# Kernel optimization log

Measured on AMD Instinct MI355X. Metric: run time of the kernel, lower is better.

The kernel has to match this reference:

```python
import jax, jax.numpy as jnp
import numpy as np

B, C, H, W, KS = 64, 128, 36, 100, 9
WSCALE = 0.02  # < 1/sqrt(C*KS) to keep the additive recurrence stable


def setup_inputs() -> dict:
    key = jax.random.key(0)
    kx, kd, ku, kr, kl = jax.random.split(key, 5)
    return {
        "x": jax.random.normal(kx, (B, C, H, W), dtype=jnp.float32),
        "w_d": jax.random.normal(kd, (C, C, KS), dtype=jnp.float32) * WSCALE,
        "w_u": jax.random.normal(ku, (C, C, KS), dtype=jnp.float32) * WSCALE,
        "w_r": jax.random.normal(kr, (C, C, KS), dtype=jnp.float32) * WSCALE,
        "w_l": jax.random.normal(kl, (C, C, KS), dtype=jnp.float32) * WSCALE,
    }


def _conv1d(z, w):
    # z: [B, C, L], w: [Cout, Cin, ks], SAME padding (matches padding=ks//2, bias=False)
    ks = w.shape[-1]
    return jax.lax.conv_general_dilated(
        z, w, window_strides=(1,), padding=[(ks // 2, ks // 2)],
        dimension_numbers=("NCH", "OIH", "NCH"))


def _scan_dir(x, w, axis, reverse):
    # singleDURL: out[0] = slice[0]; out[i] = slice[i] + relu(conv(out[i-1]))
    xs = jnp.moveaxis(x, axis, 0)  # [L, B, C, M]
    if reverse:
        xs = xs[::-1]

    def step(carry, s):
        nxt = s + jax.nn.relu(_conv1d(carry, w))
        return nxt, nxt

    _, outs = jax.lax.scan(step, xs[0], xs[1:])
    outs = jnp.concatenate([xs[:1], outs], axis=0)
    if reverse:
        outs = outs[::-1]
    return jnp.moveaxis(outs, 0, axis)


def reference(x, w_d, w_u, w_r, w_l):
    # allDURL: D (down, scan over H, 1xks conv over W), U (up), R (right, scan over W,
    # ksx1 conv over H), L (left)
    x = _scan_dir(x, w_d, axis=2, reverse=False)
    x = _scan_dir(x, w_u, axis=2, reverse=True)
    x = _scan_dir(x, w_r, axis=3, reverse=False)
    x = _scan_dir(x, w_l, axis=3, reverse=True)
    return x
```

## Files before the change

kernel.cpp:

```cpp
#include <hip/hip_runtime.h>

#define Bn 64
#define Cn 128
#define Hn 36
#define Wn 100
#define KSn 9

#define B_STRIDE (Cn * Hn * Wn)
#define C_STRIDE (Hn * Wn)

#define WH_CHUNK 80
#define WW_CHUNK 40
#define WH_SIZE (16 * Cn * WH_CHUNK)
#define WW_SIZE (32 * Cn * WW_CHUNK)

__global__ void __launch_bounds__(256) k_copy(const float4* __restrict__ s,
                                              float4* __restrict__ d, int n4) {
  int i = blockIdx.x * 256 + threadIdx.x;
  if (i < n4) d[i] = s[i];
}

__global__ void __launch_bounds__(256) k_prep_h(const float* __restrict__ w,
                                                float* __restrict__ o) {
  int i = blockIdx.x * 256 + threadIdx.x;
  if (i >= 16 * Cn * 72) return;
  int k = i % 9, j = (i / 9) % 8, ci = (i / 72) % Cn, cog = i / (72 * Cn);
  o[(cog * Cn + ci) * WH_CHUNK + j * 9 + k] = w[((cog * 8 + j) * Cn + ci) * KSn + k];
}
__global__ void __launch_bounds__(256) k_prep_w(const float* __restrict__ w,
                                                float* __restrict__ o) {
  int i = blockIdx.x * 256 + threadIdx.x;
  if (i >= 32 * Cn * 36) return;
  int k = i % 9, j = (i / 9) % 4, ci = (i / 36) % Cn, coq = i / (36 * Cn);
  o[(coq * Cn + ci) * WW_CHUNK + j * 9 + k] = w[((coq * 4 + j) * Cn + ci) * KSn + k];
}

__global__ void __launch_bounds__(256) k_hstep2(float* __restrict__ buf,
                                                const float* __restrict__ wp,
                                                int hp, int hc) {
  __shared__ float prev[Cn][Wn + 8];
  const int b = blockIdx.x;
  const int t = threadIdx.x;

  const float* rb = buf + ((size_t)b * Cn * Hn + hp) * Wn;
  for (int g = t; g < Cn * (Wn / 4); g += 256) {
    int ci = g / 25, wq = g % 25;
    float4 v = *(const float4*)(rb + (size_t)ci * C_STRIDE + wq * 4);
    *(float4*)&prev[ci][4 + wq * 4] = v;
  }
  for (int g = t; g < Cn * 8; g += 256) {
    int ci = g >> 3, s = g & 7;
    prev[ci][(s < 4) ? s : (Wn + s)] = 0.f;
  }
  __syncthreads();

  const int w = t & 127;
  if (w >= Wn) return;
  const int cog = blockIdx.y * 2 + __builtin_amdgcn_readfirstlane(t >> 7);

  float acc[8] = {0.f, 0.f, 0.f, 0.f, 0.f, 0.f, 0.f, 0.f};
  const float* wb = wp + (size_t)cog * Cn * WH_CHUNK;
#pragma unroll 2
  for (int ci = 0; ci < Cn; ++ci) {
    float p[KSn];
#pragma unroll
    for (int k = 0; k < KSn; ++k) p[k] = prev[ci][w + k];
    const float* wr = wb + ci * WH_CHUNK;
#pragma unroll
    for (int j = 0; j < 8; ++j)
#pragma unroll
      for (int k = 0; k < KSn; ++k) acc[j] = fmaf(p[k], wr[j * 9 + k], acc[j]);
  }
  float* ob = buf + ((size_t)(b * Cn + cog * 8) * Hn + hc) * Wn + w;
#pragma unroll
  for (int j = 0; j < 8; ++j) ob[(size_t)j * C_STRIDE] += fmaxf(acc[j], 0.f);
}

__global__ void __launch_bounds__(256) k_wstep2(float* __restrict__ tb,
                                                const float* __restrict__ wp,
                                                int wpos, int wc) {
  __shared__ float prev[Cn][Hn + 8];
  const int b = blockIdx.x;
  const int t = threadIdx.x;

  const float* cb = tb + ((size_t)b * Cn * Wn + wpos) * Hn;
  for (int g = t; g < Cn * (Hn / 4); g += 256) {
    int ci = g / 9, hq = g % 9;
    float4 v = *(const float4*)(cb + (size_t)ci * C_STRIDE + hq * 4);
    *(float4*)&prev[ci][4 + hq * 4] = v;
  }
  for (int g = t; g < Cn * 8; g += 256) {
    int ci = g >> 3, s = g & 7;
    prev[ci][(s < 4) ? s : (Hn + s)] = 0.f;
  }
  __syncthreads();

  const int h = t & 63;
  if (h >= Hn) return;
  const int coq = blockIdx.y * 4 + __builtin_amdgcn_readfirstlane(t >> 6);

  float acc[4] = {0.f, 0.f, 0.f, 0.f};
  const float* wb = wp + (size_t)coq * Cn * WW_CHUNK;
#pragma unroll 2
  for (int ci = 0; ci < Cn; ++ci) {
    float p[KSn];
#pragma unroll
    for (int k = 0; k < KSn; ++k) p[k] = prev[ci][h + k];
    const float* wr = wb + ci * WW_CHUNK;
#pragma unroll
    for (int j = 0; j < 4; ++j)
#pragma unroll
      for (int k = 0; k < KSn; ++k) acc[j] = fmaf(p[k], wr[j * 9 + k], acc[j]);
  }
  float* ob = tb + ((size_t)(b * Cn + coq * 4) * Wn + wc) * Hn + h;
#pragma unroll
  for (int j = 0; j < 4; ++j) ob[(size_t)j * C_STRIDE] += fmaxf(acc[j], 0.f);
}

__global__ void __launch_bounds__(256) k_t_hw2wh(const float* __restrict__ in,
                                                 float* __restrict__ out) {
  __shared__ float tile[Hn][Wn + 1];
  const int bc = blockIdx.x;
  const float* ib = in + (size_t)bc * C_STRIDE;
  float* ob = out + (size_t)bc * C_STRIDE;
  for (int f = threadIdx.x; f < Hn * Wn; f += 256) tile[f / Wn][f % Wn] = ib[f];
  __syncthreads();
  for (int f = threadIdx.x; f < Hn * Wn; f += 256) {
    int w = f / Hn, h = f % Hn;
    ob[f] = tile[h][w];
  }
}
__global__ void __launch_bounds__(256) k_t_wh2hw(const float* __restrict__ in,
                                                 float* __restrict__ out) {
  __shared__ float tile[Hn][Wn + 1];
  const int bc = blockIdx.x;
  const float* ib = in + (size_t)bc * C_STRIDE;
  float* ob = out + (size_t)bc * C_STRIDE;
  for (int f = threadIdx.x; f < Hn * Wn; f += 256) {
    int w = f / Hn, h = f % Hn;
    tile[h][w] = ib[f];
  }
  __syncthreads();
  for (int f = threadIdx.x; f < Hn * Wn; f += 256) ob[f] = tile[f / Wn][f % Wn];
}

__global__ void __launch_bounds__(128) k_hstep(float* __restrict__ buf,
                                               const float* __restrict__ wt,
                                               int hp, int hc) {
  __shared__ float prev[Cn][Wn + 8];
  const int b = blockIdx.x;
  const int cog = blockIdx.y;
  const int t = threadIdx.x;
  const float* rb = buf + ((size_t)b * Cn * Hn + hp) * Wn;
  for (int g = t; g < Cn * (Wn / 4); g += 128) {
    int ci = g / 25, wq = g % 25;
    float4 v = *(const float4*)(rb + (size_t)ci * C_STRIDE + wq * 4);
    *(float4*)&prev[ci][4 + wq * 4] = v;
  }
  for (int g = t; g < Cn * 8; g += 128) {
    int ci = g >> 3, s = g & 7;
    prev[ci][(s < 4) ? s : (Wn + s)] = 0.f;
  }
  __syncthreads();
  if (t >= Wn) return;
  float acc[8] = {0.f, 0.f, 0.f, 0.f, 0.f, 0.f, 0.f, 0.f};
  const float* wb = wt + (size_t)cog * 8 * Cn * KSn;
  for (int ci = 0; ci < Cn; ++ci) {
    float p[KSn];
#pragma unroll
    for (int k = 0; k < KSn; ++k) p[k] = prev[ci][t + k];
#pragma unroll
    for (int j = 0; j < 8; ++j) {
      const float* w9 = wb + ((size_t)j * Cn + ci) * KSn;
#pragma unroll
      for (int k = 0; k < KSn; ++k) acc[j] = fmaf(p[k], w9[k], acc[j]);
    }
  }
  float* ob = buf + ((size_t)(b * Cn + cog * 8) * Hn + hc) * Wn + t;
#pragma unroll
  for (int j = 0; j < 8; ++j) ob[(size_t)j * C_STRIDE] += fmaxf(acc[j], 0.f);
}
__global__ void __launch_bounds__(128) k_wstep_d(float* __restrict__ buf,
                                                 const float* __restrict__ wt,
                                                 int wpos, int wc) {
  __shared__ float prev[Cn][Hn + 8];
  const int b = blockIdx.x;
  const int cog = blockIdx.y;
  const int t = threadIdx.x;
  const int h = t & 63;
  const int jb = __builtin_amdgcn_readfirstlane((t >> 6) * 4);
  for (int g = t; g < Cn * Hn; g += 128) {
    int ci = g / Hn, hh = g % Hn;
    prev[ci][4 + hh] = buf[((size_t)(b * Cn + ci) * Hn + hh) * Wn + wpos];
  }
  for (int g = t; g < Cn * 8; g += 128) {
    int ci = g >> 3, s = g & 7;
    prev[ci][(s < 4) ? s : (Hn + s)] = 0.f;
  }
  __syncthreads();
  if (h >= Hn) return;
  float acc[4] = {0.f, 0.f, 0.f, 0.f};
  const float* wb = wt + (size_t)(cog * 8 + jb) * Cn * KSn;
  for (int ci = 0; ci < Cn; ++ci) {
    float p[KSn];
#pragma unroll
    for (int k = 0; k < KSn; ++k) p[k] = prev[ci][h + k];
#pragma unroll
    for (int j = 0; j < 4; ++j) {
      const float* w9 = wb + ((size_t)j * Cn + ci) * KSn;
#pragma unroll
      for (int k = 0; k < KSn; ++k) acc[j] = fmaf(p[k], w9[k], acc[j]);
    }
  }
  float* ob = buf + ((size_t)(b * Cn + cog * 8 + jb) * Hn + h) * Wn + wc;
#pragma unroll
  for (int j = 0; j < 4; ++j) ob[(size_t)j * C_STRIDE] += fmaxf(acc[j], 0.f);
}

extern "C" void kernel_launch(void* const* d_in, const int* in_sizes, int n_in,
                              void* d_out, int out_size, void* d_ws, size_t ws_size,
                              hipStream_t stream) {
  const float* x  = (const float*)d_in[0];
  const float* wd = (const float*)d_in[1];
  const float* wu = (const float*)d_in[2];
  const float* wr = (const float*)d_in[3];
  const float* wl = (const float*)d_in[4];
  float* buf = (float*)d_out;
  const size_t nelem = (size_t)Bn * B_STRIDE;
  const size_t need = (nelem + 2 * (size_t)WH_SIZE + 2 * (size_t)WW_SIZE) * 4;

  k_copy<<<(int)(nelem / 4 + 255) / 256, 256, 0, stream>>>(
      (const float4*)x, (float4*)buf, (int)(nelem / 4));

  if (ws_size >= need) {
    float* tb  = (float*)d_ws;
    float* pwd = tb + nelem;
    float* pwu = pwd + WH_SIZE;
    float* pwr = pwu + WH_SIZE;
    float* pwl = pwr + WW_SIZE;

    k_prep_h<<<(16 * Cn * 72 + 255) / 256, 256, 0, stream>>>(wd, pwd);
    k_prep_h<<<(16 * Cn * 72 + 255) / 256, 256, 0, stream>>>(wu, pwu);
    k_prep_w<<<(32 * Cn * 36 + 255) / 256, 256, 0, stream>>>(wr, pwr);
    k_prep_w<<<(32 * Cn * 36 + 255) / 256, 256, 0, stream>>>(wl, pwl);

    dim3 gh(Bn, Cn / 16);
    for (int hh = 1; hh < Hn; ++hh)
      k_hstep2<<<gh, 256, 0, stream>>>(buf, pwd, hh - 1, hh);
    for (int hh = Hn - 2; hh >= 0; --hh)
      k_hstep2<<<gh, 256, 0, stream>>>(buf, pwu, hh + 1, hh);

    k_t_hw2wh<<<Bn * Cn, 256, 0, stream>>>(buf, tb);
    dim3 gw(Bn, Cn / 16);
    for (int ww = 1; ww < Wn; ++ww)
      k_wstep2<<<gw, 256, 0, stream>>>(tb, pwr, ww - 1, ww);
    for (int ww = Wn - 2; ww >= 0; --ww)
      k_wstep2<<<gw, 256, 0, stream>>>(tb, pwl, ww + 1, ww);
    k_t_wh2hw<<<Bn * Cn, 256, 0, stream>>>(tb, buf);
  } else {
    dim3 g8(Bn, Cn / 8);
    for (int hh = 1; hh < Hn; ++hh)
      k_hstep<<<g8, 128, 0, stream>>>(buf, wd, hh - 1, hh);
    for (int hh = Hn - 2; hh >= 0; --hh)
      k_hstep<<<g8, 128, 0, stream>>>(buf, wu, hh + 1, hh);
    for (int ww = 1; ww < Wn; ++ww)
      k_wstep_d<<<g8, 128, 0, stream>>>(buf, wr, ww - 1, ww);
    for (int ww = Wn - 2; ww >= 0; --ww)
      k_wstep_d<<<g8, 128, 0, stream>>>(buf, wl, ww + 1, ww);
  }
}
```

Before: 10.19 ms.

## Register-tile step kernels with LDS-staged weights and split-K reduction

Rewrites the per-row and per-column recurrence step kernels so each thread computes a 4-channel by 4/5-position register tile. Weights are re-laid out once and staged in chunks through shared memory, with a register double-buffer prefetching the next chunk. The W-direction kernel also splits the input channels across the four wavefronts and reduces the partial sums through shared memory. The goal is more FMAs per load, fewer redundant global weight reads, and fewer blocks per step (grid of 64x4 instead of 64x8). In exchange it adds more __syncthreads, higher register pressure and lower parallelism per launch.

Measured after the change: 11.03 ms. 1.08x slower.

```diff
diff --git a/kernel.cpp b/kernel.cpp
--- a/kernel.cpp
+++ b/kernel.cpp
@@ -9,10 +9,7 @@
 #define B_STRIDE (Cn * Hn * Wn)
 #define C_STRIDE (Hn * Wn)
 
-#define WH_CHUNK 80
-#define WW_CHUNK 40
-#define WH_SIZE (16 * Cn * WH_CHUNK)
-#define WW_SIZE (32 * Cn * WW_CHUNK)
+#define PW_SIZE (Cn * Cn * KSn)
 
 __global__ void __launch_bounds__(256) k_copy(const float4* __restrict__ s,
                                               float4* __restrict__ d, int n4) {
@@ -20,101 +17,198 @@
   if (i < n4) d[i] = s[i];
 }
 
-__global__ void __launch_bounds__(256) k_prep_h(const float* __restrict__ w,
-                                                float* __restrict__ o) {
+__global__ void __launch_bounds__(256) k_prep3(const float* __restrict__ w,
+                                               float* __restrict__ o) {
   int i = blockIdx.x * 256 + threadIdx.x;
-  if (i >= 16 * Cn * 72) return;
-  int k = i % 9, j = (i / 9) % 8, ci = (i / 72) % Cn, cog = i / (72 * Cn);
-  o[(cog * Cn + ci) * WH_CHUNK + j * 9 + k] = w[((cog * 8 + j) * Cn + ci) * KSn + k];
-}
-__global__ void __launch_bounds__(256) k_prep_w(const float* __restrict__ w,
-                                                float* __restrict__ o) {
-  int i = blockIdx.x * 256 + threadIdx.x;
-  if (i >= 32 * Cn * 36) return;
-  int k = i % 9, j = (i / 9) % 4, ci = (i / 36) % Cn, coq = i / (36 * Cn);
-  o[(coq * Cn + ci) * WW_CHUNK + j * 9 + k] = w[((coq * 4 + j) * Cn + ci) * KSn + k];
-}
-
-__global__ void __launch_bounds__(256) k_hstep2(float* __restrict__ buf,
+  if (i >= PW_SIZE) return;
+  int k = i % 9;
+  int j = (i / 9) & 3;
+  int coset = (i / 36) & 7;
+  int ci = (i / 288) & 127;
+  int coq = i / 36864;
+  o[i] = w[((coq * 32 + coset * 4 + j) * Cn + ci) * KSn + k];
+}
+
+__global__ void __launch_bounds__(256) k_hstep3(float* __restrict__ buf,
                                                 const float* __restrict__ wp,
                                                 int hp, int hc) {
   __shared__ float prev[Cn][Wn + 8];
-  const int b = blockIdx.x;
-  const int t = threadIdx.x;
+  __shared__ float wch[8][8][36];
+  const int b = blockIdx.x, coq = blockIdx.y, t = threadIdx.x;
+  const int coset = t & 7;
+  const int wgrp = t >> 3;
+  const int w0r = wgrp * 4;
+  const int w0 = (w0r > 96) ? 96 : w0r;
 
   const float* rb = buf + ((size_t)b * Cn * Hn + hp) * Wn;
-  for (int g = t; g < Cn * (Wn / 4); g += 256) {
+  for (int g = t; g < Cn * 25; g += 256) {
     int ci = g / 25, wq = g % 25;
-    float4 v = *(const float4*)(rb + (size_t)ci * C_STRIDE + wq * 4);
-    *(float4*)&prev[ci][4 + wq * 4] = v;
+    *(float4*)&prev[ci][4 + wq * 4] = *(const float4*)(rb + (size_t)ci * C_STRIDE + wq * 4);
   }
   for (int g = t; g < Cn * 8; g += 256) {
     int ci = g >> 3, s = g & 7;
     prev[ci][(s < 4) ? s : (Wn + s)] = 0.f;
   }
-  __syncthreads();
-
-  const int w = t & 127;
-  if (w >= Wn) return;
-  const int cog = blockIdx.y * 2 + __builtin_amdgcn_readfirstlane(t >> 7);
-
-  float acc[8] = {0.f, 0.f, 0.f, 0.f, 0.f, 0.f, 0.f, 0.f};
-  const float* wb = wp + (size_t)cog * Cn * WH_CHUNK;
+
+  const float* wsrc = wp + (size_t)coq * (Cn * 288);
+  float4 wstage[3];
+  {
+    const float4* s4 = (const float4*)wsrc;
+#pragma unroll
+    for (int r = 0; r < 3; ++r) {
+      int g = t + 256 * r;
+      if (g < 576) wstage[r] = s4[g];
+    }
+  }
+
+  float acc[4][4] = {};
+  float4* d4 = (float4*)&wch[0][0][0];
+  for (int c = 0; c < 16; ++c) {
+    __syncthreads();
+#pragma unroll
+    for (int r = 0; r < 3; ++r) {
+      int g = t + 256 * r;
+      if (g < 576) d4[g] = wstage[r];
+    }
+    __syncthreads();
+    if (c < 15) {
+      const float4* s4 = (const float4*)(wsrc + (c + 1) * 2304);
+#pragma unroll
+      for (int r = 0; r < 3; ++r) {
+        int g = t + 256 * r;
+        if (g < 576) wstage[r] = s4[g];
+      }
+    }
 #pragma unroll 2
-  for (int ci = 0; ci < Cn; ++ci) {
-    float p[KSn];
-#pragma unroll
-    for (int k = 0; k < KSn; ++k) p[k] = prev[ci][w + k];
-    const float* wr = wb + ci * WH_CHUNK;
-#pragma unroll
-    for (int j = 0; j < 8; ++j)
-#pragma unroll
-      for (int k = 0; k < KSn; ++k) acc[j] = fmaf(p[k], wr[j * 9 + k], acc[j]);
-  }
-  float* ob = buf + ((size_t)(b * Cn + cog * 8) * Hn + hc) * Wn + w;
-#pragma unroll
-  for (int j = 0; j < 8; ++j) ob[(size_t)j * C_STRIDE] += fmaxf(acc[j], 0.f);
-}
-
-__global__ void __launch_bounds__(256) k_wstep2(float* __restrict__ tb,
+    for (int c8 = 0; c8 < 8; ++c8) {
+      const int ci = c * 8 + c8;
+      float p[12];
+#pragma unroll
+      for (int q = 0; q < 12; ++q) p[q] = prev[ci][w0 + q];
+      const float* wr = &wch[c8][coset][0];
+      float wreg[36];
+#pragma unroll
+      for (int r = 0; r < 36; ++r) wreg[r] = wr[r];
+#pragma unroll
+      for (int j = 0; j < 4; ++j)
+#pragma unroll
+        for (int k = 0; k < KSn; ++k) {
+          const float wv = wreg[j * 9 + k];
+#pragma unroll
+          for (int i = 0; i < 4; ++i) acc[j][i] = fmaf(p[i + k], wv, acc[j][i]);
+        }
+    }
+  }
+
+  if (w0r <= 96) {
+    float* ob = buf + ((size_t)(b * Cn + coq * 32 + coset * 4) * Hn + hc) * Wn + w0;
+#pragma unroll
+    for (int j = 0; j < 4; ++j) {
+      float4* op = (float4*)(ob + (size_t)j * C_STRIDE);
+      float4 o = *op;
+      o.x += fmaxf(acc[j][0], 0.f);
+      o.y += fmaxf(acc[j][1], 0.f);
+      o.z += fmaxf(acc[j][2], 0.f);
+      o.w += fmaxf(acc[j][3], 0.f);
+      *op = o;
+    }
+  }
+}
+
+__global__ void __launch_bounds__(256) k_wstep3(float* __restrict__ tb,
                                                 const float* __restrict__ wp,
                                                 int wpos, int wc) {
   __shared__ float prev[Cn][Hn + 8];
-  const int b = blockIdx.x;
-  const int t = threadIdx.x;
+  __shared__ float wch[4][8][8][36];
+  const int b = blockIdx.x, coq = blockIdx.y, t = threadIdx.x;
+  const int wv = t >> 6, l = t & 63;
+  const int coset = l & 7, hgrp = l >> 3;
+  const int h0r = hgrp * 5;
+  const int h0 = (h0r > 31) ? 31 : h0r;
 
   const float* cb = tb + ((size_t)b * Cn * Wn + wpos) * Hn;
-  for (int g = t; g < Cn * (Hn / 4); g += 256) {
+  for (int g = t; g < Cn * 9; g += 256) {
     int ci = g / 9, hq = g % 9;
-    float4 v = *(const float4*)(cb + (size_t)ci * C_STRIDE + hq * 4);
-    *(float4*)&prev[ci][4 + hq * 4] = v;
+    *(float4*)&prev[ci][4 + hq * 4] = *(const float4*)(cb + (size_t)ci * C_STRIDE + hq * 4);
   }
   for (int g = t; g < Cn * 8; g += 256) {
     int ci = g >> 3, s = g & 7;
     prev[ci][(s < 4) ? s : (Hn + s)] = 0.f;
   }
-  __syncthreads();
-
-  const int h = t & 63;
-  if (h >= Hn) return;
-  const int coq = blockIdx.y * 4 + __builtin_amdgcn_readfirstlane(t >> 6);
-
-  float acc[4] = {0.f, 0.f, 0.f, 0.f};
-  const float* wb = wp + (size_t)coq * Cn * WW_CHUNK;
+
+  const float* wsrc = wp + (size_t)coq * (Cn * 288);
+  float4 wstage[9];
+#pragma unroll
+  for (int r = 0; r < 9; ++r) {
+    int g = t + 256 * r;
+    int gw = g / 576, rem = g % 576;
+    wstage[r] = *((const float4*)wsrc + (size_t)(gw * 32) * 72 + rem);
+  }
+
+  float acc[4][5] = {};
+  float4* d4 = (float4*)&wch[0][0][0][0];
+  for (int c = 0; c < 4; ++c) {
+    __syncthreads();
+#pragma unroll
+    for (int r = 0; r < 9; ++r) d4[t + 256 * r] = wstage[r];
+    __syncthreads();
+    if (c < 3) {
+#pragma unroll
+      for (int r = 0; r < 9; ++r) {
+        int g = t + 256 * r;
+        int gw = g / 576, rem = g % 576;
+        wstage[r] = *((const float4*)wsrc + (size_t)(gw * 32 + (c + 1) * 8) * 72 + rem);
+      }
+    }
 #pragma unroll 2
-  for (int ci = 0; ci < Cn; ++ci) {
-    float p[KSn];
-#pragma unroll
-    for (int k = 0; k < KSn; ++k) p[k] = prev[ci][h + k];
-    const float* wr = wb + ci * WW_CHUNK;
-#pragma unroll
-    for (int j = 0; j < 4; ++j)
-#pragma unroll
-      for (int k = 0; k < KSn; ++k) acc[j] = fmaf(p[k], wr[j * 9 + k], acc[j]);
-  }
-  float* ob = tb + ((size_t)(b * Cn + coq * 4) * Wn + wc) * Hn + h;
-#pragma unroll
-  for (int j = 0; j < 4; ++j) ob[(size_t)j * C_STRIDE] += fmaxf(acc[j], 0.f);
+    for (int c8 = 0; c8 < 8; ++c8) {
+      const int ci = wv * 32 + c * 8 + c8;
+      float p[13];
+#pragma unroll
+      for (int q = 0; q < 13; ++q) p[q] = prev[ci][h0 + q];
+      const float* wr = &wch[wv][c8][coset][0];
+      float wreg[36];
+#pragma unroll
+      for (int r = 0; r < 36; ++r) wreg[r] = wr[r];
+#pragma unroll
+      for (int j = 0; j < 4; ++j)
+#pragma unroll
+        for (int k = 0; k < KSn; ++k) {
+          const float wvv = wreg[j * 9 + k];
+#pragma unroll
+          for (int i = 0; i < 5; ++i) acc[j][i] = fmaf(p[i + k], wvv, acc[j][i]);
+        }
+    }
+  }
+
+  __syncthreads();
+  float* red = &wch[0][0][0][0];
+#pragma unroll
+  for (int j = 0; j < 4; ++j)
+#pragma unroll
+    for (int i = 0; i < 5; ++i) red[(wv * 64 + l) * 20 + j * 5 + i] = acc[j][i];
+  __syncthreads();
+  {
+    const int oh = t & 7, oc = t >> 3;
+    const int rj = oc & 3, rcs = oc >> 2;
+    const int rl = oh * 8 + rcs;
+    const int oh0r = oh * 5;
+    const int oh0 = (oh0r > 31) ? 31 : oh0r;
+    float v[5];
+#pragma unroll
+    for (int i = 0; i < 5; ++i) v[i] = red[rl * 20 + rj * 5 + i];
+#pragma unroll
+    for (int w2 = 1; w2 < 4; ++w2)
+#pragma unroll
+      for (int i = 0; i < 5; ++i) v[i] += red[(w2 * 64 + rl) * 20 + rj * 5 + i];
+    const int co = coq * 32 + rcs * 4 + rj;
+    float* ob = tb + ((size_t)(b * Cn + co) * Wn + wc) * Hn;
+#pragma unroll
+    for (int i = 0; i < 5; ++i) {
+      const int h = oh0 + i;
+      if (h >= oh0r && h < Hn) ob[h] += fmaxf(v[i], 0.f);
+    }
+  }
 }
 
 __global__ void __launch_bounds__(256) k_t_hw2wh(const float* __restrict__ in,
@@ -220,6 +314,7 @@
 extern "C" void kernel_launch(void* const* d_in, const int* in_sizes, int n_in,
                               void* d_out, int out_size, void* d_ws, size_t ws_size,
                               hipStream_t stream) {
+  (void)in_sizes; (void)n_in; (void)out_size;
   const float* x  = (const float*)d_in[0];
   const float* wd = (const float*)d_in[1];
   const float* wu = (const float*)d_in[2];
@@ -227,7 +322,7 @@
   const float* wl = (const float*)d_in[4];
   float* buf = (float*)d_out;
   const size_t nelem = (size_t)Bn * B_STRIDE;
-  const size_t need = (nelem + 2 * (size_t)WH_SIZE + 2 * (size_t)WW_SIZE) * 4;
+  const size_t need = (nelem + 4 * (size_t)PW_SIZE) * 4;
 
   k_copy<<<(int)(nelem / 4 + 255) / 256, 256, 0, stream>>>(
       (const float4*)x, (float4*)buf, (int)(nelem / 4));
@@ -235,27 +330,27 @@
   if (ws_size >= need) {
     float* tb  = (float*)d_ws;
     float* pwd = tb + nelem;
-    float* pwu = pwd + WH_SIZE;
-    float* pwr = pwu + WH_SIZE;
-    float* pwl = pwr + WW_SIZE;
-
-    k_prep_h<<<(16 * Cn * 72 + 255) / 256, 256, 0, stream>>>(wd, pwd);
-    k_prep_h<<<(16 * Cn * 72 + 255) / 256, 256, 0, stream>>>(wu, pwu);
-    k_prep_w<<<(32 * Cn * 36 + 255) / 256, 256, 0, stream>>>(wr, pwr);
-    k_prep_w<<<(32 * Cn * 36 + 255) / 256, 256, 0, stream>>>(wl, pwl);
-
-    dim3 gh(Bn, Cn / 16);
+    float* pwu = pwd + PW_SIZE;
+    float* pwr = pwu + PW_SIZE;
+    float* pwl = pwr + PW_SIZE;
+
+    const int pg = (PW_SIZE + 255) / 256;
+    k_prep3<<<pg, 256, 0, stream>>>(wd, pwd);
+    k_prep3<<<pg, 256, 0, stream>>>(wu, pwu);
+    k_prep3<<<pg, 256, 0, stream>>>(wr, pwr);
+    k_prep3<<<pg, 256, 0, stream>>>(wl, pwl);
+
+    dim3 g4(Bn, 4);
     for (int hh = 1; hh < Hn; ++hh)
-      k_hstep2<<<gh, 256, 0, stream>>>(buf, pwd, hh - 1, hh);
+      k_hstep3<<<g4, 256, 0, stream>>>(buf, pwd, hh - 1, hh);
     for (int hh = Hn - 2; hh >= 0; --hh)
-      k_hstep2<<<gh, 256, 0, stream>>>(buf, pwu, hh + 1, hh);
+      k_hstep3<<<g4, 256, 0, stream>>>(buf, pwu, hh + 1, hh);
 
     k_t_hw2wh<<<Bn * Cn, 256, 0, stream>>>(buf, tb);
-    dim3 gw(Bn, Cn / 16);
     for (int ww = 1; ww < Wn; ++ww)
-      k_wstep2<<<gw, 256, 0, stream>>>(tb, pwr, ww - 1, ww);
+      k_wstep3<<<g4, 256, 0, stream>>>(tb, pwr, ww - 1, ww);
     for (int ww = Wn - 2; ww >= 0; --ww)
-      k_wstep2<<<gw, 256, 0, stream>>>(tb, pwl, ww + 1, ww);
+      k_wstep3<<<g4, 256, 0, stream>>>(tb, pwl, ww + 1, ww);
     k_t_wh2hw<<<Bn * Cn, 256, 0, stream>>>(tb, buf);
   } else {
     dim3 g8(Bn, Cn / 8);
```

## Fuse per-step scan launches into persistent kernels with per-batch atomic barriers

Applied to the files above, without the earlier changes.

Replaces the ~268 per-step kernel launches of the H and W scans with two persistent kernels of 256 blocks (512 threads each). The blocks for one batch element synchronise each step through a global atomic counter barrier. The goal is to remove launch overhead and the global sync between steps. In exchange it depends on all 256 blocks being co-resident, since the barrier would deadlock otherwise. It also lowers per-block parallelism, uses spin-wait polling, and relies on caches being coherent across workgroups.

After: 11.54 ms. 13.2% more time.

```diff
diff --git a/kernel.cpp b/kernel.cpp
--- a/kernel.cpp
+++ b/kernel.cpp
@@ -18,6 +18,11 @@
                                               float4* __restrict__ d, int n4) {
   int i = blockIdx.x * 256 + threadIdx.x;
   if (i < n4) d[i] = s[i];
+}
+
+__global__ void __launch_bounds__(256) k_zero(unsigned* p, int n) {
+  int i = blockIdx.x * 256 + threadIdx.x;
+  if (i < n) p[i] = 0u;
 }
 
 __global__ void __launch_bounds__(256) k_prep_h(const float* __restrict__ w,
@@ -35,86 +40,130 @@
   o[(coq * Cn + ci) * WW_CHUNK + j * 9 + k] = w[((coq * 4 + j) * Cn + ci) * KSn + k];
 }
 
-__global__ void __launch_bounds__(256) k_hstep2(float* __restrict__ buf,
-                                                const float* __restrict__ wp,
-                                                int hp, int hc) {
+__device__ __forceinline__ void bbar(unsigned* c, unsigned target) {
+  __syncthreads();
+  if (threadIdx.x == 0) {
+    __hip_atomic_fetch_add(c, 1u, __ATOMIC_RELEASE, __HIP_MEMORY_SCOPE_AGENT);
+    while (__hip_atomic_load(c, __ATOMIC_RELAXED, __HIP_MEMORY_SCOPE_AGENT) <
+           target)
+      __builtin_amdgcn_s_sleep(1);
+    __builtin_amdgcn_fence(__ATOMIC_ACQUIRE, "agent");
+  }
+  __syncthreads();
+}
+
+__global__ void __launch_bounds__(512, 1) k_hfused(float* __restrict__ buf,
+                                                   const float* __restrict__ pwd,
+                                                   const float* __restrict__ pwu,
+                                                   unsigned* __restrict__ ctr) {
   __shared__ float prev[Cn][Wn + 8];
-  const int b = blockIdx.x;
+  const int bid = blockIdx.x;
+  const int b = bid & 63;
+  const int coq = bid >> 6;
   const int t = threadIdx.x;
-
-  const float* rb = buf + ((size_t)b * Cn * Hn + hp) * Wn;
-  for (int g = t; g < Cn * (Wn / 4); g += 256) {
-    int ci = g / 25, wq = g % 25;
-    float4 v = *(const float4*)(rb + (size_t)ci * C_STRIDE + wq * 4);
-    *(float4*)&prev[ci][4 + wq * 4] = v;
-  }
-  for (int g = t; g < Cn * 8; g += 256) {
-    int ci = g >> 3, s = g & 7;
-    prev[ci][(s < 4) ? s : (Wn + s)] = 0.f;
-  }
-  __syncthreads();
-
   const int w = t & 127;
-  if (w >= Wn) return;
-  const int cog = blockIdx.y * 2 + __builtin_amdgcn_readfirstlane(t >> 7);
-
-  float acc[8] = {0.f, 0.f, 0.f, 0.f, 0.f, 0.f, 0.f, 0.f};
-  const float* wb = wp + (size_t)cog * Cn * WH_CHUNK;
+  const int plane = __builtin_amdgcn_readfirstlane(t >> 7);
+  const int cog = coq * 4 + plane;
+  unsigned* myc = ctr + b;
+  unsigned gen = 0;
+
+  for (int phase = 0; phase < 2; ++phase) {
+    const float* wp = phase ? pwu : pwd;
+    const float* wb = wp + (size_t)cog * Cn * WH_CHUNK;
+    for (int s = 0; s < Hn - 1; ++s) {
+      const int hc = phase ? (Hn - 2 - s) : (1 + s);
+      const int hp = phase ? (hc + 1) : (hc - 1);
+
+      const float* rb = buf + ((size_t)b * Cn * Hn + hp) * Wn;
+      for (int g = t; g < Cn * 25; g += 512) {
+        int ci = g / 25, wq = g % 25;
+        *(float4*)&prev[ci][4 + wq * 4] =
+            *(const float4*)(rb + (size_t)ci * C_STRIDE + wq * 4);
+      }
+      for (int g = t; g < Cn * 8; g += 512) {
+        int ci = g >> 3, sp = g & 7;
+        prev[ci][(sp < 4) ? sp : (Wn + sp)] = 0.f;
+      }
+      __syncthreads();
+
+      if (w < Wn) {
+        float acc[8] = {0.f, 0.f, 0.f, 0.f, 0.f, 0.f, 0.f, 0.f};
 #pragma unroll 2
-  for (int ci = 0; ci < Cn; ++ci) {
-    float p[KSn];
-#pragma unroll
-    for (int k = 0; k < KSn; ++k) p[k] = prev[ci][w + k];
-    const float* wr = wb + ci * WH_CHUNK;
-#pragma unroll
-    for (int j = 0; j < 8; ++j)
-#pragma unroll
-      for (int k = 0; k < KSn; ++k) acc[j] = fmaf(p[k], wr[j * 9 + k], acc[j]);
-  }
-  float* ob = buf + ((size_t)(b * Cn + cog * 8) * Hn + hc) * Wn + w;
-#pragma unroll
-  for (int j = 0; j < 8; ++j) ob[(size_t)j * C_STRIDE] += fmaxf(acc[j], 0.f);
-}
-
-__global__ void __launch_bounds__(256) k_wstep2(float* __restrict__ tb,
-                                                const float* __restrict__ wp,
-                                                int wpos, int wc) {
+        for (int ci = 0; ci < Cn; ++ci) {
+          float p[KSn];
+#pragma unroll
+          for (int k = 0; k < KSn; ++k) p[k] = prev[ci][w + k];
+          const float* wr = wb + ci * WH_CHUNK;
+#pragma unroll
+          for (int j = 0; j < 8; ++j)
+#pragma unroll
+            for (int k = 0; k < KSn; ++k) acc[j] = fmaf(p[k], wr[j * 9 + k], acc[j]);
+        }
+        float* ob = buf + ((size_t)(b * Cn + cog * 8) * Hn + hc) * Wn + w;
+#pragma unroll
+        for (int j = 0; j < 8; ++j) ob[(size_t)j * C_STRIDE] += fmaxf(acc[j], 0.f);
+      }
+      ++gen;
+      bbar(myc, gen * 4u);
+    }
+  }
+}
+
+__global__ void __launch_bounds__(512, 1) k_wfused(float* __restrict__ tb,
+                                                   const float* __restrict__ pwr,
+                                                   const float* __restrict__ pwl,
+                                                   unsigned* __restrict__ ctr) {
   __shared__ float prev[Cn][Hn + 8];
-  const int b = blockIdx.x;
+  const int bid = blockIdx.x;
+  const int b = bid & 63;
+  const int coq = bid >> 6;
   const int t = threadIdx.x;
-
-  const float* cb = tb + ((size_t)b * Cn * Wn + wpos) * Hn;
-  for (int g = t; g < Cn * (Hn / 4); g += 256) {
-    int ci = g / 9, hq = g % 9;
-    float4 v = *(const float4*)(cb + (size_t)ci * C_STRIDE + hq * 4);
-    *(float4*)&prev[ci][4 + hq * 4] = v;
-  }
-  for (int g = t; g < Cn * 8; g += 256) {
-    int ci = g >> 3, s = g & 7;
-    prev[ci][(s < 4) ? s : (Hn + s)] = 0.f;
-  }
-  __syncthreads();
-
   const int h = t & 63;
-  if (h >= Hn) return;
-  const int coq = blockIdx.y * 4 + __builtin_amdgcn_readfirstlane(t >> 6);
-
-  float acc[4] = {0.f, 0.f, 0.f, 0.f};
-  const float* wb = wp + (size_t)coq * Cn * WW_CHUNK;
+  const int v = __builtin_amdgcn_readfirstlane(t >> 6);
+  const int quadg = coq * 8 + v;
+  unsigned* myc = ctr + b;
+  unsigned gen = 0;
+
+  for (int phase = 0; phase < 2; ++phase) {
+    const float* wp = phase ? pwl : pwr;
+    const float* wb = wp + (size_t)quadg * Cn * WW_CHUNK;
+    for (int s = 0; s < Wn - 1; ++s) {
+      const int wc = phase ? (Wn - 2 - s) : (1 + s);
+      const int wpos = phase ? (wc + 1) : (wc - 1);
+
+      const float* cb = tb + ((size_t)b * Cn * Wn + wpos) * Hn;
+      for (int g = t; g < Cn * 9; g += 512) {
+        int ci = g / 9, hq = g % 9;
+        *(float4*)&prev[ci][4 + hq * 4] =
+            *(const float4*)(cb + (size_t)ci * C_STRIDE + hq * 4);
+      }
+      for (int g = t; g < Cn * 8; g += 512) {
+        int ci = g >> 3, sp = g & 7;
+        prev[ci][(sp < 4) ? sp : (Hn + sp)] = 0.f;
+      }
+      __syncthreads();
+
+      if (h < Hn) {
+        float acc[4] = {0.f, 0.f, 0.f, 0.f};
 #pragma unroll 2
-  for (int ci = 0; ci < Cn; ++ci) {
-    float p[KSn];
-#pragma unroll
-    for (int k = 0; k < KSn; ++k) p[k] = prev[ci][h + k];
-    const float* wr = wb + ci * WW_CHUNK;
-#pragma unroll
-    for (int j = 0; j < 4; ++j)
-#pragma unroll
-      for (int k = 0; k < KSn; ++k) acc[j] = fmaf(p[k], wr[j * 9 + k], acc[j]);
-  }
-  float* ob = tb + ((size_t)(b * Cn + coq * 4) * Wn + wc) * Hn + h;
-#pragma unroll
-  for (int j = 0; j < 4; ++j) ob[(size_t)j * C_STRIDE] += fmaxf(acc[j], 0.f);
+        for (int ci = 0; ci < Cn; ++ci) {
+          float p[KSn];
+#pragma unroll
+          for (int k = 0; k < KSn; ++k) p[k] = prev[ci][h + k];
+          const float* wr = wb + ci * WW_CHUNK;
+#pragma unroll
+          for (int j = 0; j < 4; ++j)
+#pragma unroll
+            for (int k = 0; k < KSn; ++k) acc[j] = fmaf(p[k], wr[j * 9 + k], acc[j]);
+        }
+        float* ob = tb + ((size_t)(b * Cn + quadg * 4) * Wn + wc) * Hn + h;
+#pragma unroll
+        for (int j = 0; j < 4; ++j) ob[(size_t)j * C_STRIDE] += fmaxf(acc[j], 0.f);
+      }
+      ++gen;
+      bbar(myc, gen * 4u);
+    }
+  }
 }
 
 __global__ void __launch_bounds__(256) k_t_hw2wh(const float* __restrict__ in,
@@ -126,8 +175,8 @@
   for (int f = threadIdx.x; f < Hn * Wn; f += 256) tile[f / Wn][f % Wn] = ib[f];
   __syncthreads();
   for (int f = threadIdx.x; f < Hn * Wn; f += 256) {
-    int w = f / Hn, h = f % Hn;
-    ob[f] = tile[h][w];
+    int w = f / Hn, hh = f % Hn;
+    ob[f] = tile[hh][w];
   }
 }
 __global__ void __launch_bounds__(256) k_t_wh2hw(const float* __restrict__ in,
@@ -137,8 +186,8 @@
   const float* ib = in + (size_t)bc * C_STRIDE;
   float* ob = out + (size_t)bc * C_STRIDE;
   for (int f = threadIdx.x; f < Hn * Wn; f += 256) {
-    int w = f / Hn, h = f % Hn;
-    tile[h][w] = ib[f];
+    int w = f / Hn, hh = f % Hn;
+    tile[hh][w] = ib[f];
   }
   __syncthreads();
   for (int f = threadIdx.x; f < Hn * Wn; f += 256) ob[f] = tile[f / Wn][f % Wn];
@@ -154,8 +203,8 @@
   const float* rb = buf + ((size_t)b * Cn * Hn + hp) * Wn;
   for (int g = t; g < Cn * (Wn / 4); g += 128) {
     int ci = g / 25, wq = g % 25;
-    float4 v = *(const float4*)(rb + (size_t)ci * C_STRIDE + wq * 4);
-    *(float4*)&prev[ci][4 + wq * 4] = v;
+    float4 vv = *(const float4*)(rb + (size_t)ci * C_STRIDE + wq * 4);
+    *(float4*)&prev[ci][4 + wq * 4] = vv;
   }
   for (int g = t; g < Cn * 8; g += 128) {
     int ci = g >> 3, s = g & 7;
@@ -220,6 +269,7 @@
 extern "C" void kernel_launch(void* const* d_in, const int* in_sizes, int n_in,
                               void* d_out, int out_size, void* d_ws, size_t ws_size,
                               hipStream_t stream) {
+  (void)in_sizes; (void)n_in; (void)out_size;
   const float* x  = (const float*)d_in[0];
   const float* wd = (const float*)d_in[1];
   const float* wu = (const float*)d_in[2];
@@ -227,7 +277,7 @@
   const float* wl = (const float*)d_in[4];
   float* buf = (float*)d_out;
   const size_t nelem = (size_t)Bn * B_STRIDE;
-  const size_t need = (nelem + 2 * (size_t)WH_SIZE + 2 * (size_t)WW_SIZE) * 4;
+  const size_t need = (nelem + 2 * (size_t)WH_SIZE + 2 * (size_t)WW_SIZE) * 4 + 512;
 
   k_copy<<<(int)(nelem / 4 + 255) / 256, 256, 0, stream>>>(
       (const float4*)x, (float4*)buf, (int)(nelem / 4));
@@ -238,24 +288,17 @@
     float* pwu = pwd + WH_SIZE;
     float* pwr = pwu + WH_SIZE;
     float* pwl = pwr + WW_SIZE;
-
+    unsigned* ctr = (unsigned*)(pwl + WW_SIZE);
+
+    k_zero<<<1, 256, 0, stream>>>(ctr, 128);
     k_prep_h<<<(16 * Cn * 72 + 255) / 256, 256, 0, stream>>>(wd, pwd);
     k_prep_h<<<(16 * Cn * 72 + 255) / 256, 256, 0, stream>>>(wu, pwu);
     k_prep_w<<<(32 * Cn * 36 + 255) / 256, 256, 0, stream>>>(wr, pwr);
     k_prep_w<<<(32 * Cn * 36 + 255) / 256, 256, 0, stream>>>(wl, pwl);
 
-    dim3 gh(Bn, Cn / 16);
-    for (int hh = 1; hh < Hn; ++hh)
-      k_hstep2<<<gh, 256, 0, stream>>>(buf, pwd, hh - 1, hh);
-    for (int hh = Hn - 2; hh >= 0; --hh)
-      k_hstep2<<<gh, 256, 0, stream>>>(buf, pwu, hh + 1, hh);
-
+    k_hfused<<<256, 512, 0, stream>>>(buf, pwd, pwu, ctr);
     k_t_hw2wh<<<Bn * Cn, 256, 0, stream>>>(buf, tb);
-    dim3 gw(Bn, Cn / 16);
-    for (int ww = 1; ww < Wn; ++ww)
-      k_wstep2<<<gw, 256, 0, stream>>>(tb, pwr, ww - 1, ww);
-    for (int ww = Wn - 2; ww >= 0; --ww)
-      k_wstep2<<<gw, 256, 0, stream>>>(tb, pwl, ww + 1, ww);
+    k_wfused<<<256, 512, 0, stream>>>(tb, pwr, pwl, ctr + 64);
     k_t_wh2hw<<<Bn * Cn, 256, 0, stream>>>(tb, buf);
   } else {
     dim3 g8(Bn, Cn / 8);
```
